# Performance work log

Measured on AMD Instinct MI355X. Metric: run time of the kernel, lower is better.

The kernel has to match this reference:

```python
import jax, jax.numpy as jnp
import numpy as np

BS, HW, HIDDEN, TOK, NTOK = 32, 1024, 256, 768, 2048


def setup_inputs() -> dict:
    key = jax.random.key(0)
    ks = jax.random.split(key, 6)
    s = 0.02  # init scale for weights
    return {
        "src": jax.random.normal(ks[0], (HW, BS, HIDDEN), jnp.float32),
        "codebook": jax.random.normal(ks[1], (NTOK, TOK), jnp.float32),
        "w_head": jax.random.normal(ks[2], (TOK, HIDDEN), jnp.float32) * s,
        "w_tail": jax.random.normal(ks[3], (HIDDEN, TOK), jnp.float32) * s,
        "w_pos": jax.random.normal(ks[4], (TOK, TOK), jnp.float32) * s,
        "b_pos": jnp.zeros((TOK,), jnp.float32),
        "w_gate": jax.random.normal(ks[5], (2, 2 * TOK), jnp.float32) * s,
        "h": 32,
        "w": 32,
    }


def reference(src, codebook, w_head, w_tail, w_pos, b_pos, w_gate, h, w):
    N, bs, hidden = src.shape  # [num_visu_token, bs, hidden_dim]
    tok = codebook.shape[1]
    # permute(1,2,0).view(bs,-1,h,w)
    x = jnp.transpose(src, (1, 2, 0)).reshape(bs, hidden, h, w)
    # conv_head: 1x1 conv, no bias
    xq = jnp.einsum("bchw,oc->bohw", x, w_head)  # [bs, tok, h, w]
    # raw-memory reshape, matches torch .view(-1, token_dim)
    flat = xq.reshape(-1, tok)  # [bs*h*w, tok]
    d = (
        jnp.sum(flat * flat, axis=1, keepdims=True)
        - 2.0 * flat @ codebook.T
        + jnp.sum(codebook * codebook, axis=1)[None, :]
    )
    indices = jnp.argmin(d, axis=1)  # [bs*h*w]
    quantized = codebook[indices]  # gather
    # straight-through estimator
    quantized = flat + jax.lax.stop_gradient(quantized - flat)
    # pos_align linear
    quantized = quantized @ w_pos.T + b_pos
    # view(bs, N, tok).permute(0,2,1).view(bs,-1,h,w)
    emb = jnp.transpose(quantized.reshape(bs, N, tok), (0, 2, 1)).reshape(bs, tok, h, w)
    # gated fusion
    gate_in = jnp.concatenate([emb, xq], axis=1)  # [bs, 2*tok, h, w]
    scores = jax.nn.softmax(jnp.einsum("bchw,oc->bohw", gate_in, w_gate), axis=1)
    fused = emb * scores[:, 0:1] + xq * scores[:, 1:2]
    # conv_tail 1x1, then flatten(2).permute(2,0,1)
    out = jnp.einsum("bchw,oc->bohw", fused, w_tail)  # [bs, hidden, h, w]
    out = jnp.transpose(out.reshape(bs, hidden, -1), (2, 0, 1))  # [h*w, bs, hidden]
    return out, indices
```

## Files before the change

kernel.cpp:

```cpp
#include <hip/hip_runtime.h>
#include <cstdint>

#define BSZ 32
#define NVIS 1024
#define HID 256
#define TOKD 768
#define NCODE 2048
#define NPIX 32768

typedef unsigned short u16;
typedef _Float16 half8 __attribute__((ext_vector_type(8)));
typedef unsigned short ushort8 __attribute__((ext_vector_type(8)));
typedef unsigned short u16x4 __attribute__((ext_vector_type(4)));
using f32x4 = __attribute__((ext_vector_type(4))) float;

#define AS1 __attribute__((address_space(1)))
#define AS3 __attribute__((address_space(3)))

__device__ __forceinline__ f32x4 mfmaF16(half8 a, half8 b, f32x4 c) {
  return __builtin_amdgcn_mfma_f32_16x16x32_f16(a, b, c, 0, 0, 0);
}

__device__ __forceinline__ unsigned long long pack_key(float d, int idx) {
  unsigned int b = __float_as_uint(d);
  b = (b & 0x80000000u) ? ~b : (b | 0x80000000u);
  return ((unsigned long long)b << 32) | (unsigned int)idx;
}

__device__ __forceinline__ void split16(float v, u16& h, u16& l) {
  union { _Float16 f; u16 u; } a, b;
  a.f = (_Float16)v;
  float hf = (float)a.f;
  b.f = (_Float16)(v - hf);
  h = a.u; l = b.u;
}

__global__ __launch_bounds__(256)
void prep1(const float* __restrict__ cb, const float* __restrict__ wh,
           const float* __restrict__ wt, const float* __restrict__ wp,
           const float* __restrict__ wg, const float* __restrict__ bp,
           const float* __restrict__ src,
           u16* __restrict__ cbh, u16* __restrict__ cbl,
           u16* __restrict__ whh, u16* __restrict__ whl,
           u16* __restrict__ srch, u16* __restrict__ srcl,
           float* __restrict__ cbn, float* __restrict__ Mm, float* __restrict__ uv,
           float* __restrict__ Gt, float* __restrict__ g2,
           float* __restrict__ ct0, float* __restrict__ cg,
           unsigned long long* __restrict__ keys) {
  const int bid = blockIdx.x, tid = threadIdx.x;
  if (bid < 6144) {
    int i = bid*256 + tid;
    u16 h, l; split16(cb[i], h, l);
    cbh[i] = h; cbl[i] = l;
  } else if (bid < 6912) {
    int i = (bid - 6144)*256 + tid;
    u16 h, l; split16(wh[i], h, l);
    whh[i] = h; whl[i] = l;
  } else if (bid < 7424) {
    int n = (bid - 6912)*4 + (tid >> 6);
    int lane = tid & 63;
    float a = 0.f;
#pragma unroll
    for (int i = 0; i < 12; ++i) { float v = cb[(long)n*TOKD + lane + 64*i]; a += v*v; }
#pragma unroll
    for (int off = 32; off; off >>= 1) a += __shfl_down(a, off);
    if (lane == 0) cbn[n] = a;
  } else if (bid < 7680) {
    int c2 = bid - 7424, c1 = tid;
    float acc = 0.f;
    for (int t = 0; t < TOKD; ++t) acc += wh[t*HID + c1] * wt[(long)c2*TOKD + t];
    Mm[c1*HID + c2] = acc;
  } else if (bid < 7682) {
    int o = bid - 7680, c1 = tid;
    float acc = 0.f;
    for (int t = 0; t < TOKD; ++t) acc += wh[t*HID + c1] * wg[o*(2*TOKD) + TOKD + t];
    uv[o*HID + c1] = acc;
  } else if (bid < 8450) {
    int rbid = bid - 7682;
    int c = rbid & 255, part = rbid >> 8;
    int tp = part*256 + tid;
    float acc = 0.f;
    for (int t = 0; t < TOKD; ++t) acc += wt[(long)c*TOKD + t] * wp[(long)t*TOKD + tp];
    Gt[(long)tp*HID + c] = acc;
  } else if (bid < 8453) {
    int tp = (bid - 8450)*256 + tid;
    float a0 = 0.f, a1 = 0.f;
    for (int t = 0; t < TOKD; ++t) {
      float wv = wp[(long)t*TOKD + tp];
      a0 += wv * wg[t];
      a1 += wv * wg[2*TOKD + t];
    }
    g2[tp] = a0; g2[TOKD + tp] = a1;
  } else if (bid < 8454) {
    int c = tid;
    float a = 0.f;
    for (int t = 0; t < TOKD; ++t) a += bp[t] * wt[(long)c*TOKD + t];
    ct0[c] = a;
  } else if (bid < 8455) {
    int o = tid >> 6, lane = tid & 63;
    if (o < 2) {
      float a = 0.f;
      for (int t = lane; t < TOKD; t += 64) a += bp[t] * wg[o*(2*TOKD) + t];
#pragma unroll
      for (int off = 32; off; off >>= 1) a += __shfl_down(a, off);
      if (lane == 0) cg[o] = a;
    }
  } else if (bid < 8583) {
    int i = (bid - 8455)*256 + tid;
    keys[i] = ~0ULL;
  } else {
    long i0 = (long)(bid - 8583)*2048 + tid*8;
    float4 v0 = *(const float4*)(src + i0);
    float4 v1 = *(const float4*)(src + i0 + 4);
    float vv[8] = {v0.x, v0.y, v0.z, v0.w, v1.x, v1.y, v1.z, v1.w};
    ushort8 hv, lv;
#pragma unroll
    for (int j = 0; j < 8; ++j) { u16 hs, ls; split16(vv[j], hs, ls); hv[j] = hs; lv[j] = ls; }
    *(ushort8*)(srch + i0) = hv;
    *(ushort8*)(srcl + i0) = lv;
  }
}

__global__ __launch_bounds__(256)
void prep2(const float* __restrict__ cb, const float* __restrict__ Gt,
           const float* __restrict__ ct0, const float* __restrict__ g2,
           const float* __restrict__ cg, float* __restrict__ tc,
           float* __restrict__ gA) {
  __shared__ float cbs[8][TOKD];
  const int n0 = blockIdx.x * 8, tid = threadIdx.x;
  for (int i = tid; i < 8*TOKD; i += 256) cbs[i / TOKD][i % TOKD] = cb[(long)n0*TOKD + i];
  __syncthreads();
  float acc[8] = {};
  for (int t = 0; t < TOKD; ++t) {
    float gv = Gt[(long)t*HID + tid];
#pragma unroll
    for (int i = 0; i < 8; ++i) acc[i] += cbs[i][t] * gv;
  }
  float c0v = ct0[tid];
#pragma unroll
  for (int i = 0; i < 8; ++i) tc[(long)(n0+i)*HID + tid] = acc[i] + c0v;
  {
    int i = tid >> 5, l32 = tid & 31;
    float a0 = 0.f, a1 = 0.f;
    for (int t = l32; t < TOKD; t += 32) {
      float cv = cbs[i][t];
      a0 += cv * g2[t];
      a1 += cv * g2[TOKD + t];
    }
#pragma unroll
    for (int off = 16; off; off >>= 1) { a0 += __shfl_down(a0, off); a1 += __shfl_down(a1, off); }
    if (l32 == 0) { gA[n0+i] = a0 + cg[0]; gA[NCODE + n0+i] = a1 + cg[1]; }
  }
}

__global__ __launch_bounds__(256)
void head_mfma(const u16* __restrict__ whh, const u16* __restrict__ whl,
               const u16* __restrict__ srch, const u16* __restrict__ srcl,
               u16* __restrict__ xqh, u16* __restrict__ xql) {
  __shared__ u16 SM[32768] __attribute__((aligned(16)));
  u16* Ah = SM;
  u16* Al = SM + 8192;
  u16* Bh = SM + 16384;
  u16* Bl = SM + 24576;
  const int tid = threadIdx.x, lane = tid & 63, w = tid >> 6;
  const int n = lane & 15, q = lane >> 4;
  const int rh = w & 1, ch = w >> 1;
  const int obase = blockIdx.x * 128, pbase = blockIdx.y * 128, b = blockIdx.z;

  auto stageA = [&](int kc, int buf) {
#pragma unroll
    for (int is = 0; is < 2; ++is) {
      int c = is*256 + tid;
      int t = c >> 6, qq = (c >> 4) & 3, nn = c & 15;
      long off = (long)(obase + t*16 + nn)*HID + kc*32 + qq*8;
      __builtin_amdgcn_global_load_lds((AS1 void*)(whh + off),
          (AS3 void*)&Ah[buf*4096 + c*8], 16, 0, 0);
      __builtin_amdgcn_global_load_lds((AS1 void*)(whl + off),
          (AS3 void*)&Al[buf*4096 + c*8], 16, 0, 0);
    }
  };
  auto stageB = [&](int kc, int buf) {
#pragma unroll
    for (int is = 0; is < 2; ++is) {
      int c = is*256 + tid;
      int r = ((c >> 6) << 4) + (c & 15), qq = (c >> 4) & 3;
      long off = ((long)(pbase + r)*BSZ + b)*HID + kc*32 + qq*8;
      __builtin_amdgcn_global_load_lds((AS1 void*)(srch + off),
          (AS3 void*)&Bh[buf*4096 + c*8], 16, 0, 0);
      __builtin_amdgcn_global_load_lds((AS1 void*)(srcl + off),
          (AS3 void*)&Bl[buf*4096 + c*8], 16, 0, 0);
    }
  };

  f32x4 acc[4][4];
#pragma unroll
  for (int i = 0; i < 4; ++i)
#pragma unroll
    for (int j = 0; j < 4; ++j) acc[i][j] = (f32x4){0.f, 0.f, 0.f, 0.f};

  stageA(0, 0); stageB(0, 0);
  __syncthreads();

  for (int kt = 0; kt < HID/32; ++kt) {
    const int buf = kt & 1;
    if (kt + 1 < HID/32) { stageA(kt + 1, buf ^ 1); stageB(kt + 1, buf ^ 1); }
    half8 af[4][2], bf[4][2];
#pragma unroll
    for (int rt = 0; rt < 4; ++rt) {
      int idx = buf*4096 + ((rh*4 + rt)*64 + q*16 + n)*8;
      af[rt][0] = *(const half8*)&Ah[idx];
      af[rt][1] = *(const half8*)&Al[idx];
    }
#pragma unroll
    for (int ct = 0; ct < 4; ++ct) {
      int idx = buf*4096 + ((ch*4 + ct)*64 + q*16 + n)*8;
      bf[ct][0] = *(const half8*)&Bh[idx];
      bf[ct][1] = *(const half8*)&Bl[idx];
    }
#pragma unroll
    for (int rt = 0; rt < 4; ++rt)
#pragma unroll
      for (int ct = 0; ct < 4; ++ct) {
        acc[rt][ct] = mfmaF16(af[rt][0], bf[ct][0], acc[rt][ct]);
        acc[rt][ct] = mfmaF16(af[rt][0], bf[ct][1], acc[rt][ct]);
        acc[rt][ct] = mfmaF16(af[rt][1], bf[ct][0], acc[rt][ct]);
      }
    __syncthreads();
  }

#pragma unroll
  for (int pass = 0; pass < 2; ++pass) {
    u16* dst = pass ? xql : xqh;
#pragma unroll
    for (int rt = 0; rt < 4; ++rt)
#pragma unroll
      for (int ct = 0; ct < 4; ++ct)
#pragma unroll
        for (int reg = 0; reg < 4; ++reg) {
          u16 hs, ls; split16(acc[rt][ct][reg], hs, ls);
          int ol = rh*64 + rt*16 + q*4 + reg;
          int pl = ch*64 + ct*16 + n;
          SM[ol*136 + pl] = pass ? ls : hs;
        }
    __syncthreads();
#pragma unroll
    for (int s = 0; s < 8; ++s) {
      int cc = tid*8 + s;
      int o = cc >> 4, p8 = cc & 15;
      ushort8 v = *(const ushort8*)&SM[o*136 + p8*8];
      *(ushort8*)(dst + ((long)b*TOKD + obase + o)*NVIS + pbase + p8*8) = v;
    }
    __syncthreads();
  }
}

__global__ __launch_bounds__(256)
void retile(u16* __restrict__ bufH, u16* __restrict__ bufL) {
  __shared__ u16 T[96*136] __attribute__((aligned(16)));
  const long tile = blockIdx.x;
  const int tid = threadIdx.x;
#pragma unroll
  for (int pass = 0; pass < 2; ++pass) {
    u16* buf = pass ? bufL : bufH;
    if (pass) __syncthreads();
#pragma unroll
    for (int i = 0; i < 6; ++i) {
      int g = i*256 + tid;
      int row = g / 96, c16 = g % 96;
      ushort8 v = *(const ushort8*)(buf + tile*12288 + row*768 + c16*8);
      *(ushort8*)&T[c16*136 + row*8] = v;
    }
    __syncthreads();
#pragma unroll
    for (int i = 0; i < 6; ++i) {
      int g = i*256 + tid;
      int kc = g >> 6, lp = g & 63;
      int q = lp >> 4, n = lp & 15;
      ushort8 v = *(const ushort8*)&T[(kc*4 + q)*136 + n*8];
      *(ushort8*)(buf + tile*12288 + (long)kc*512 + lp*8) = v;
    }
  }
}

__global__ __launch_bounds__(256, 2)
void vq_mfma(const u16* __restrict__ xqh, const u16* __restrict__ xql,
             const u16* __restrict__ cbh, const u16* __restrict__ cbl,
             const float* __restrict__ cbn, unsigned long long* __restrict__ keys) {
  __shared__ u16 SM[32768] __attribute__((aligned(16)));
  const int bid = blockIdx.x;
  const int xcd = bid & 7, slot = bid >> 3;
  const int rowBlk = xcd * 16 + (slot >> 4);
  const int codeBlk = slot & 15;
  const int rowTile0 = rowBlk * 16;
  const int codeTile0 = codeBlk * 8;
  const int tid = threadIdx.x, lane = tid & 63, w = tid >> 6;
  const int n = lane & 15, q = lane >> 4;

  const u16* paH = xqh + (size_t)(rowTile0 + 4*w) * 12288 + (size_t)n*768 + q*8;
  const u16* paL = xql + (size_t)(rowTile0 + 4*w) * 12288 + (size_t)n*768 + q*8;
  const u16* pbH0 = cbh + (size_t)(codeTile0 + 2*w) * 12288 + lane*8;
  const u16* pbL0 = cbl + (size_t)(codeTile0 + 2*w) * 12288 + lane*8;
  const int bChunk = (2*w)*512 + lane*8;

  auto STAGE_B = [&](int kk, int buf) {
    const u16* ph = pbH0 + kk*512;
    const u16* pl = pbL0 + kk*512;
    u16* lh_ = &SM[buf*8192 + bChunk];
    u16* ll_ = &SM[buf*8192 + 4096 + bChunk];
    __builtin_amdgcn_global_load_lds((AS1 void*)ph,           (AS3 void*)lh_,         16, 0, 0);
    __builtin_amdgcn_global_load_lds((AS1 void*)(ph + 12288), (AS3 void*)(lh_ + 512), 16, 0, 0);
    __builtin_amdgcn_global_load_lds((AS1 void*)pl,           (AS3 void*)ll_,         16, 0, 0);
    __builtin_amdgcn_global_load_lds((AS1 void*)(pl + 12288), (AS3 void*)(ll_ + 512), 16, 0, 0);
  };

  f32x4 acc[4][8];
#pragma unroll
  for (int a = 0; a < 4; ++a)
#pragma unroll
    for (int b2 = 0; b2 < 8; ++b2) acc[a][b2] = (f32x4){0.f, 0.f, 0.f, 0.f};

  half8 AH0[4], AH1[4], AL[4], Bf[8];

  STAGE_B(0, 0); STAGE_B(1, 1);
#pragma unroll
  for (int i = 0; i < 4; ++i) AH0[i] = *(const half8*)(paH + (size_t)i*12288);
  asm volatile("s_waitcnt vmcnt(0)" ::: "memory");
  asm volatile("s_barrier" ::: "memory");

#define VQ_REGION(KK, CUR, NXT)                                              \
  {                                                                          \
    const int kk_ = (KK);                                                    \
    const int pf_ = (kk_ + 2 > 23) ? 23 : kk_ + 2;                           \
    const int pa_ = (kk_ + 1 > 23) ? 23 : kk_ + 1;                           \
    STAGE_B(pf_, (kk_ + 2) & 3);                                  \
    _Pragma("unroll")                                                        \
    for (int i = 0; i < 4; ++i) AL[i]  = *(const half8*)(paL + kk_*32 + (size_t)i*12288); \
    _Pragma("unroll")                                                        \
    for (int i = 0; i < 4; ++i) NXT[i] = *(const half8*)(paH + pa_*32 + (size_t)i*12288); \
    const int bb = (kk_ & 3)*8192;                                           \
    _Pragma("unroll")                                                        \
    for (int ct = 0; ct < 8; ++ct) Bf[ct] = *(const half8*)&SM[bb + ct*512 + lane*8]; \
    __builtin_amdgcn_s_setprio(1);                                           \
    _Pragma("unroll")                                                        \
    for (int rt = 0; rt < 4; ++rt)                                           \
      _Pragma("unroll")                                                      \
      for (int ct = 0; ct < 8; ++ct)                                         \
        acc[rt][ct] = mfmaF16(CUR[rt], Bf[ct], acc[rt][ct]);         \
    _Pragma("unroll")                                                        \
    for (int rt = 0; rt < 4; ++rt)                                           \
      _Pragma("unroll")                                                      \
      for (int ct = 0; ct < 8; ++ct)                                         \
        acc[rt][ct] = mfmaF16(AL[rt], Bf[ct], acc[rt][ct]);          \
    __builtin_amdgcn_s_setprio(0);                                           \
    _Pragma("unroll")                                                        \
    for (int ct = 0; ct < 8; ++ct) Bf[ct] = *(const half8*)&SM[bb + 4096 + ct*512 + lane*8]; \
    __builtin_amdgcn_s_setprio(1);                                           \
    _Pragma("unroll")                                                        \
    for (int rt = 0; rt < 4; ++rt)                                           \
      _Pragma("unroll")                                                      \
      for (int ct = 0; ct < 8; ++ct)                                         \
        acc[rt][ct] = mfmaF16(CUR[rt], Bf[ct], acc[rt][ct]);         \
    __builtin_amdgcn_s_setprio(0);                                           \
    asm volatile("s_waitcnt vmcnt(12)" ::: "memory");  \
    asm volatile("s_barrier" ::: "memory");            \
  }

#pragma unroll 1
  for (int h2 = 0; h2 < 12; ++h2) {
    VQ_REGION(2*h2,     AH0, AH1);
    VQ_REGION(2*h2 + 1, AH1, AH0);
  }
#undef VQ_REGION

  float cbv[8];
#pragma unroll
  for (int ct = 0; ct < 8; ++ct) cbv[ct] = cbn[(codeTile0 + ct)*16 + n];
#pragma unroll
  for (int rt = 0; rt < 4; ++rt) {
#pragma unroll
    for (int reg = 0; reg < 4; ++reg) {
      float bd = 3.4e38f; int bi = 0;
#pragma unroll
      for (int ct = 0; ct < 8; ++ct) {
        float d = cbv[ct] - 2.0f * acc[rt][ct][reg];
        int code = (codeTile0 + ct)*16 + n;
        if (d < bd) { bd = d; bi = code; }
      }
      unsigned long long k = pack_key(bd, bi);
      unsigned long long v;
      v = __shfl_xor(k, 1); k = (v < k) ? v : k;
      v = __shfl_xor(k, 2); k = (v < k) ? v : k;
      v = __shfl_xor(k, 4); k = (v < k) ? v : k;
      v = __shfl_xor(k, 8); k = (v < k) ? v : k;
      if (n == 0) {
        int row = (rowTile0 + 4*w + rt)*16 + q*4 + reg;
        atomicMin(&keys[row], k);
      }
    }
  }
}

__global__ __launch_bounds__(256)
void fuse_out(const float* __restrict__ src, const unsigned long long* __restrict__ keys,
              const float* __restrict__ gA, const float* __restrict__ uvec,
              const float* __restrict__ Mm, const float* __restrict__ tailcode,
              float* __restrict__ out, float* __restrict__ outIdx) {
  __shared__ float ss[32][257];
  __shared__ float s0s[32];
  __shared__ int ids[32];
  const int tid = threadIdx.x;
  const int rb = blockIdx.x * 32;
  const int b = rb >> 10;
  const int p0 = rb & 1023;
#pragma unroll
  for (int qq = 0; qq < 32; ++qq)
    ss[qq][tid] = src[(long)(p0 + qq) * (BSZ*HID) + b*HID + tid];
  if (tid < 32) {
    unsigned long long u = keys[rb + tid];
    int id = (int)(unsigned int)(u & 0xFFFFFFFFull);
    ids[tid] = id;
    outIdx[rb + tid] = (float)id;
  }
  __syncthreads();
  {
    const int wv = tid >> 6, lane = tid & 63;
    for (int qq = 0; qq < 8; ++qq) {
      int qp = wv*8 + qq;
      float a0 = 0.f, a1 = 0.f;
#pragma unroll
      for (int i = 0; i < 4; ++i) {
        float v = ss[qp][lane + 64*i];
        a0 += v * uvec[lane + 64*i];
        a1 += v * uvec[HID + lane + 64*i];
      }
#pragma unroll
      for (int off = 32; off; off >>= 1) { a0 += __shfl_down(a0, off); a1 += __shfl_down(a1, off); }
      if (lane == 0) {
        int id = ids[qp];
        float l0 = gA[id] + a0;
        float l1 = gA[NCODE + id] + a1;
        s0s[qp] = 1.0f / (1.0f + expf(l1 - l0));
      }
    }
  }
  __syncthreads();
  const int qg = tid >> 5, cg = tid & 31;
  const int q0 = qg * 4, c0 = cg * 8;
  float acc[4][8] = {};
  for (int cp = 0; cp < HID; ++cp) {
    float4 m0 = *(const float4*)(Mm + cp*HID + c0);
    float4 m1 = *(const float4*)(Mm + cp*HID + c0 + 4);
    float mm[8] = {m0.x,m0.y,m0.z,m0.w,m1.x,m1.y,m1.z,m1.w};
#pragma unroll
    for (int i = 0; i < 4; ++i) {
      float sv = ss[q0+i][cp];
#pragma unroll
      for (int j = 0; j < 8; ++j) acc[i][j] += sv * mm[j];
    }
  }
#pragma unroll
  for (int i = 0; i < 4; ++i) {
    int qp = q0 + i;
    int id = ids[qp];
    float s0 = s0s[qp], s1 = 1.0f - s0;
    const float* tc = tailcode + (long)id*HID + c0;
    float* op = out + (long)(p0+qp)*(BSZ*HID) + b*HID + c0;
    float4 o0, o1;
    o0.x = s0*tc[0] + s1*acc[i][0]; o0.y = s0*tc[1] + s1*acc[i][1];
    o0.z = s0*tc[2] + s1*acc[i][2]; o0.w = s0*tc[3] + s1*acc[i][3];
    o1.x = s0*tc[4] + s1*acc[i][4]; o1.y = s0*tc[5] + s1*acc[i][5];
    o1.z = s0*tc[6] + s1*acc[i][6]; o1.w = s0*tc[7] + s1*acc[i][7];
    *(float4*)(op) = o0; *(float4*)(op+4) = o1;
  }
}

extern "C" void kernel_launch(void* const* d_in, const int* in_sizes, int n_in,
                              void* d_out, int out_size, void* d_ws, size_t ws_size,
                              hipStream_t stream) {
  const float* src    = (const float*)d_in[0];
  const float* cb     = (const float*)d_in[1];
  const float* w_head = (const float*)d_in[2];
  const float* w_tail = (const float*)d_in[3];
  const float* w_pos  = (const float*)d_in[4];
  const float* b_pos  = (const float*)d_in[5];
  const float* w_gate = (const float*)d_in[6];
  float* out = (float*)d_out;

  char* wsp = (char*)d_ws;
  size_t off = 0;
  auto alloc = [&](size_t bytes) {
    off = (off + 255) & ~(size_t)255;
    void* p = wsp + off; off += bytes; return p;
  };
  u16* xqh = (u16*)alloc((size_t)BSZ*TOKD*NVIS*2);
  u16* xql = (u16*)alloc((size_t)BSZ*TOKD*NVIS*2);
  u16* cbh = (u16*)alloc((size_t)NCODE*TOKD*2);
  u16* cbl = (u16*)alloc((size_t)NCODE*TOKD*2);
  u16* whh = (u16*)alloc((size_t)TOKD*HID*2);
  u16* whl = (u16*)alloc((size_t)TOKD*HID*2);
  u16* srch = (u16*)alloc((size_t)NVIS*BSZ*HID*2);
  u16* srcl = (u16*)alloc((size_t)NVIS*BSZ*HID*2);
  float* cbn      = (float*)alloc((size_t)NCODE*4);
  float* Gt       = (float*)alloc((size_t)TOKD*HID*4);
  float* g2       = (float*)alloc((size_t)2*TOKD*4);
  float* ct0      = (float*)alloc((size_t)HID*4);
  float* cg       = (float*)alloc((size_t)2*4);
  float* tailcode = (float*)alloc((size_t)NCODE*HID*4);
  float* gA       = (float*)alloc((size_t)2*NCODE*4);
  float* Mm       = (float*)alloc((size_t)HID*HID*4);
  float* uvec     = (float*)alloc((size_t)2*HID*4);
  unsigned long long* keys = (unsigned long long*)alloc((size_t)NPIX*8);
  (void)ws_size; (void)in_sizes; (void)n_in; (void)out_size;

  prep1<<<12679, 256, 0, stream>>>(cb, w_head, w_tail, w_pos, w_gate, b_pos, src,
                                   cbh, cbl, whh, whl, srch, srcl,
                                   cbn, Mm, uvec, Gt, g2, ct0, cg, keys);
  retile<<<NCODE/16, 256, 0, stream>>>(cbh, cbl);
  prep2<<<NCODE/8, 256, 0, stream>>>(cb, Gt, ct0, g2, cg, tailcode, gA);

  head_mfma<<<dim3(TOKD/128, NVIS/128, BSZ), 256, 0, stream>>>(whh, whl, srch, srcl,
                                                               xqh, xql);

  vq_mfma<<<2048, 256, 0, stream>>>(xqh, xql, cbh, cbl, cbn, keys);

  fuse_out<<<NPIX/32, 256, 0, stream>>>(src, keys, gA, uvec, Mm, tailcode,
                                        out, out + (size_t)NVIS*BSZ*HID);
}
```

Before: 619.4 us.

## Prefetch low A fragments a step ahead and merge retile into prep2

The VQ MFMA inner loop now double-buffers the low-half A fragments (AL0/AL1) the same way as the high half, so both are loaded one k-step ahead instead of loading AL just before use. The B fragments are read from shared memory in two halves of four, which halves the Bf registers held at once. The separate retile kernel is folded into prep2 as extra blocks, removing one kernel launch and its serialization. The trade-offs are more A registers live per wave and more outstanding global loads, which interact with the fixed vmcnt(12) wait count.

New measurement: 628.6 us. No clear change (+1.5%).

```diff
diff --git a/kernel.cpp b/kernel.cpp
--- a/kernel.cpp
+++ b/kernel.cpp
@@ -125,9 +125,37 @@
 void prep2(const float* __restrict__ cb, const float* __restrict__ Gt,
            const float* __restrict__ ct0, const float* __restrict__ g2,
            const float* __restrict__ cg, float* __restrict__ tc,
-           float* __restrict__ gA) {
+           float* __restrict__ gA,
+           u16* __restrict__ cbh, u16* __restrict__ cbl) {
+  const int tid = threadIdx.x;
+  if (blockIdx.x >= NCODE/8) {
+    __shared__ u16 T[96*136] __attribute__((aligned(16)));
+    const long tile = blockIdx.x - NCODE/8;
+#pragma unroll
+    for (int pass = 0; pass < 2; ++pass) {
+      u16* buf = pass ? cbl : cbh;
+      if (pass) __syncthreads();
+#pragma unroll
+      for (int i = 0; i < 6; ++i) {
+        int g = i*256 + tid;
+        int row = g / 96, c16 = g % 96;
+        ushort8 v = *(const ushort8*)(buf + tile*12288 + row*768 + c16*8);
+        *(ushort8*)&T[c16*136 + row*8] = v;
+      }
+      __syncthreads();
+#pragma unroll
+      for (int i = 0; i < 6; ++i) {
+        int g = i*256 + tid;
+        int kc = g >> 6, lp = g & 63;
+        int q = lp >> 4, n = lp & 15;
+        ushort8 v = *(const ushort8*)&T[(kc*4 + q)*136 + n*8];
+        *(ushort8*)(buf + tile*12288 + (long)kc*512 + lp*8) = v;
+      }
+    }
+    return;
+  }
   __shared__ float cbs[8][TOKD];
-  const int n0 = blockIdx.x * 8, tid = threadIdx.x;
+  const int n0 = blockIdx.x * 8;
   for (int i = tid; i < 8*TOKD; i += 256) cbs[i / TOKD][i % TOKD] = cb[(long)n0*TOKD + i];
   __syncthreads();
   float acc[8] = {};
@@ -254,34 +282,6 @@
   }
 }
 
-__global__ __launch_bounds__(256)
-void retile(u16* __restrict__ bufH, u16* __restrict__ bufL) {
-  __shared__ u16 T[96*136] __attribute__((aligned(16)));
-  const long tile = blockIdx.x;
-  const int tid = threadIdx.x;
-#pragma unroll
-  for (int pass = 0; pass < 2; ++pass) {
-    u16* buf = pass ? bufL : bufH;
-    if (pass) __syncthreads();
-#pragma unroll
-    for (int i = 0; i < 6; ++i) {
-      int g = i*256 + tid;
-      int row = g / 96, c16 = g % 96;
-      ushort8 v = *(const ushort8*)(buf + tile*12288 + row*768 + c16*8);
-      *(ushort8*)&T[c16*136 + row*8] = v;
-    }
-    __syncthreads();
-#pragma unroll
-    for (int i = 0; i < 6; ++i) {
-      int g = i*256 + tid;
-      int kc = g >> 6, lp = g & 63;
-      int q = lp >> 4, n = lp & 15;
-      ushort8 v = *(const ushort8*)&T[(kc*4 + q)*136 + n*8];
-      *(ushort8*)(buf + tile*12288 + (long)kc*512 + lp*8) = v;
-    }
-  }
-}
-
 __global__ __launch_bounds__(256, 2)
 void vq_mfma(const u16* __restrict__ xqh, const u16* __restrict__ xql,
              const u16* __restrict__ cbh, const u16* __restrict__ cbl,
@@ -319,56 +319,66 @@
 #pragma unroll
     for (int b2 = 0; b2 < 8; ++b2) acc[a][b2] = (f32x4){0.f, 0.f, 0.f, 0.f};
 
-  half8 AH0[4], AH1[4], AL[4], Bf[8];
+  half8 AH0[4], AH1[4], AL0[4], AL1[4], Bf[4];
 
   STAGE_B(0, 0); STAGE_B(1, 1);
 #pragma unroll
   for (int i = 0; i < 4; ++i) AH0[i] = *(const half8*)(paH + (size_t)i*12288);
+#pragma unroll
+  for (int i = 0; i < 4; ++i) AL0[i] = *(const half8*)(paL + (size_t)i*12288);
   asm volatile("s_waitcnt vmcnt(0)" ::: "memory");
   asm volatile("s_barrier" ::: "memory");
 
-#define VQ_REGION(KK, CUR, NXT)                                              \
+#define VQ_REGION(KK, CH, CL, NH, NL)                                        \
   {                                                                          \
     const int kk_ = (KK);                                                    \
     const int pf_ = (kk_ + 2 > 23) ? 23 : kk_ + 2;                           \
     const int pa_ = (kk_ + 1 > 23) ? 23 : kk_ + 1;                           \
     STAGE_B(pf_, (kk_ + 2) & 3);                                  \
     _Pragma("unroll")                                                        \
-    for (int i = 0; i < 4; ++i) AL[i]  = *(const half8*)(paL + kk_*32 + (size_t)i*12288); \
+    for (int i = 0; i < 4; ++i) NH[i] = *(const half8*)(paH + pa_*32 + (size_t)i*12288); \
     _Pragma("unroll")                                                        \
-    for (int i = 0; i < 4; ++i) NXT[i] = *(const half8*)(paH + pa_*32 + (size_t)i*12288); \
+    for (int i = 0; i < 4; ++i) NL[i] = *(const half8*)(paL + pa_*32 + (size_t)i*12288); \
     const int bb = (kk_ & 3)*8192;                                           \
     _Pragma("unroll")                                                        \
-    for (int ct = 0; ct < 8; ++ct) Bf[ct] = *(const half8*)&SM[bb + ct*512 + lane*8]; \
-    __builtin_amdgcn_s_setprio(1);                                           \
+    for (int ph_ = 0; ph_ < 2; ++ph_) {              \
+      _Pragma("unroll")                                                      \
+      for (int ct = 0; ct < 4; ++ct)                                         \
+        Bf[ct] = *(const half8*)&SM[bb + (ph_*4 + ct)*512 + lane*8];         \
+      __builtin_amdgcn_s_setprio(1);                                         \
+      _Pragma("unroll")                                                      \
+      for (int rt = 0; rt < 4; ++rt)                                         \
+        _Pragma("unroll")                                                    \
+        for (int ct = 0; ct < 4; ++ct)                                       \
+          acc[rt][ph_*4 + ct] = mfmaF16(CH[rt], Bf[ct], acc[rt][ph_*4 + ct]); \
+      _Pragma("unroll")                                                      \
+      for (int rt = 0; rt < 4; ++rt)                                         \
+        _Pragma("unroll")                                                    \
+        for (int ct = 0; ct < 4; ++ct)                                       \
+          acc[rt][ph_*4 + ct] = mfmaF16(CL[rt], Bf[ct], acc[rt][ph_*4 + ct]); \
+      __builtin_amdgcn_s_setprio(0);                                         \
+    }                                                                        \
     _Pragma("unroll")                                                        \
-    for (int rt = 0; rt < 4; ++rt)                                           \
+    for (int ph_ = 0; ph_ < 2; ++ph_) {                   \
       _Pragma("unroll")                                                      \
-      for (int ct = 0; ct < 8; ++ct)                                         \
-        acc[rt][ct] = mfmaF16(CUR[rt], Bf[ct], acc[rt][ct]);         \
-    _Pragma("unroll")                                                        \
-    for (int rt = 0; rt < 4; ++rt)                                           \
+      for (int ct = 0; ct < 4; ++ct)                                         \
+        Bf[ct] = *(const half8*)&SM[bb + 4096 + (ph_*4 + ct)*512 + lane*8];  \
+      __builtin_amdgcn_s_setprio(1);                                         \
       _Pragma("unroll")                                                      \
-      for (int ct = 0; ct < 8; ++ct)                                         \
-        acc[rt][ct] = mfmaF16(AL[rt], Bf[ct], acc[rt][ct]);          \
-    __builtin_amdgcn_s_setprio(0);                                           \
-    _Pragma("unroll")                                                        \
-    for (int ct = 0; ct < 8; ++ct) Bf[ct] = *(const half8*)&SM[bb + 4096 + ct*512 + lane*8]; \
-    __builtin_amdgcn_s_setprio(1);                                           \
-    _Pragma("unroll")                                                        \
-    for (int rt = 0; rt < 4; ++rt)                                           \
-      _Pragma("unroll")                                                      \
-      for (int ct = 0; ct < 8; ++ct)                                         \
-        acc[rt][ct] = mfmaF16(CUR[rt], Bf[ct], acc[rt][ct]);         \
-    __builtin_amdgcn_s_setprio(0);                                           \
+      for (int rt = 0; rt < 4; ++rt)                                         \
+        _Pragma("unroll")                                                    \
+        for (int ct = 0; ct < 4; ++ct)                                       \
+          acc[rt][ph_*4 + ct] = mfmaF16(CH[rt], Bf[ct], acc[rt][ph_*4 + ct]); \
+      __builtin_amdgcn_s_setprio(0);                                         \
+    }                                                                        \
     asm volatile("s_waitcnt vmcnt(12)" ::: "memory");  \
     asm volatile("s_barrier" ::: "memory");            \
   }
 
 #pragma unroll 1
   for (int h2 = 0; h2 < 12; ++h2) {
-    VQ_REGION(2*h2,     AH0, AH1);
-    VQ_REGION(2*h2 + 1, AH1, AH0);
+    VQ_REGION(2*h2,     AH0, AL0, AH1, AL1);
+    VQ_REGION(2*h2 + 1, AH1, AL1, AH0, AL0);
   }
 #undef VQ_REGION
 
@@ -515,8 +525,8 @@
   prep1<<<12679, 256, 0, stream>>>(cb, w_head, w_tail, w_pos, w_gate, b_pos, src,
                                    cbh, cbl, whh, whl, srch, srcl,
                                    cbn, Mm, uvec, Gt, g2, ct0, cg, keys);
-  retile<<<NCODE/16, 256, 0, stream>>>(cbh, cbl);
-  prep2<<<NCODE/8, 256, 0, stream>>>(cb, Gt, ct0, g2, cg, tailcode, gA);
+  prep2<<<NCODE/8 + NCODE/16, 256, 0, stream>>>(cb, Gt, ct0, g2, cg, tailcode, gA,
+                                                cbh, cbl);
 
   head_mfma<<<dim3(TOKD/128, NVIS/128, BSZ), 256, 0, stream>>>(whh, whl, srch, srcl,
                                                                xqh, xql);
```
